# Optimization experiments

Hardware: AMD Instinct MI355X
Metric: run time of the kernel (lower is better)

## Reference

```python
import jax, jax.numpy as jnp
import numpy as np

N_NODES = 100000
N_EDGES = 3200000
IN_FEAT = 128
IN_ENC = 128
HID = 256
MPNN_STEPS = 4


def setup_inputs() -> dict:
    key = jax.random.key(0)
    ks = jax.random.split(key, 12)
    x = jax.random.normal(ks[0], (N_NODES, IN_FEAT), dtype=jnp.float32)
    edge_index = jax.random.randint(ks[1], (2, N_EDGES), 0, N_NODES, dtype=jnp.int64)
    # input layer
    W_in = jax.random.normal(ks[2], (IN_ENC, IN_FEAT), dtype=jnp.float32) * (1.0 / np.sqrt(IN_FEAT))
    b_in = jax.random.normal(ks[3], (IN_ENC,), dtype=jnp.float32) * 0.01
    # MGU params (torch.randn init)
    W_f = jax.random.normal(ks[4], (HID, HID), dtype=jnp.float32)
    U_f = jax.random.normal(ks[5], (HID, HID), dtype=jnp.float32)
    b_f = jax.random.normal(ks[6], (HID,), dtype=jnp.float32)
    W_h = jax.random.normal(ks[7], (HID, HID), dtype=jnp.float32)
    U_h = jax.random.normal(ks[8], (HID, HID), dtype=jnp.float32)
    b_h = jax.random.normal(ks[9], (HID,), dtype=jnp.float32)
    # prediction layer
    W_pred = jax.random.normal(ks[10], (1, HID), dtype=jnp.float32) * (1.0 / np.sqrt(HID))
    b_pred = jax.random.normal(ks[11], (1,), dtype=jnp.float32) * 0.01
    return {"x": x, "edge_index": edge_index, "W_in": W_in, "b_in": b_in,
            "W_f": W_f, "U_f": U_f, "b_f": b_f, "W_h": W_h, "U_h": U_h, "b_h": b_h,
            "W_pred": W_pred, "b_pred": b_pred}


def _mgu_update(m, h, W_f, U_f, b_f, W_h, U_h, b_h):
    # f_t = sigmoid(m @ W_f^T + h @ U_f^T + b_f)
    f_t = jax.nn.sigmoid(m @ W_f.T + h @ U_f.T + b_f)
    h_hat = jnp.tanh(m @ W_h.T + (f_t * h) @ U_h.T + b_h)
    return (1.0 - f_t) * h + f_t * h_hat


def reference(x, edge_index, W_in, b_in, W_f, U_f, b_f, W_h, U_h, b_h, W_pred, b_pred):
    # input encoding
    h0 = jax.nn.relu(x @ W_in.T + b_in)
    # zero-pad features from IN_ENC to HID
    h = jnp.pad(h0, ((0, 0), (0, HID - IN_ENC)))
    src, dst = edge_index[0], edge_index[1]
    for _ in range(MPNN_STEPS):
        # gather neighbor (source) features, scatter-mean to destination nodes
        msg_sum = jax.ops.segment_sum(h[src], dst, num_segments=N_NODES)
        cnt = jax.ops.segment_sum(jnp.ones((src.shape[0],), dtype=h.dtype), dst,
                                  num_segments=N_NODES)
        m = msg_sum / jnp.maximum(cnt, 1.0)[:, None]
        h = _mgu_update(m, h, W_f, U_f, b_f, W_h, U_h, b_h)
    # graph-level readout: per-feature mean over nodes
    g = jnp.mean(h, axis=0)  # [HID]
    return g @ W_pred.T + b_pred  # [1]
```

## Files before the change

kernel.cpp:

```cpp
#include <hip/hip_runtime.h>
#include <hip/hip_bf16.h>
#include <math.h>

constexpr int NN = 100000;
constexpr int NE = 3200000;
constexpr int HID = 256;
constexpr int NBLK = (NN + 255) / 256;

typedef __attribute__((ext_vector_type(8))) short short8;
typedef __attribute__((ext_vector_type(4))) float floatx4;
typedef __attribute__((ext_vector_type(2))) float floatx2;
typedef __attribute__((ext_vector_type(8))) unsigned short ushort8v;

__device__ __forceinline__ float bf2f(unsigned short u) {
    unsigned int t = ((unsigned int)u) << 16;
    float f; __builtin_memcpy(&f, &t, 4); return f;
}
__device__ __forceinline__ unsigned short f2bf(float f) {
    unsigned int t; __builtin_memcpy(&t, &f, 4);
    unsigned int lsb = (t >> 16) & 1u;
    t += 0x7fffu + lsb;
    return (unsigned short)(t >> 16);
}
__device__ __forceinline__ unsigned char f2fp8(float f) {
    int pk = __builtin_amdgcn_cvt_pk_fp8_f32(f, f, 0, false);
    return (unsigned char)(pk & 0xff);
}

__device__ __forceinline__ void llds16(const void* g, void* l) {
    __builtin_amdgcn_global_load_lds(
        (const __attribute__((address_space(1))) unsigned int*)g,
        (__attribute__((address_space(3))) unsigned int*)l, 16, 0, 0);
}

__global__ void detect_i64(const int* __restrict__ ei, int* __restrict__ flag) {
    if (blockIdx.x == 0 && threadIdx.x == 0) {
        int z = 1;
        for (int i = 0; i < 64; ++i)
            if (ei[2 * i + 1] != 0) { z = 0; break; }
        *flag = z;
    }
}
__device__ __forceinline__ int load_edge(const int* ei, int is64, long long idx) {
    if (is64) return (int)(((const long long*)ei)[idx]);
    return ei[idx];
}

__global__ void zero_setup(int* __restrict__ cnt, int* __restrict__ cursor,
                           float* __restrict__ gsum) {
    int i = blockIdx.x * 256 + threadIdx.x;
    if (i < NN) { cnt[i] = 0; cursor[i] = 0; }
    if (i < HID) gsum[i] = 0.0f;
}

__global__ void conv_weights(const float* __restrict__ Wf, const float* __restrict__ Uf,
                             const float* __restrict__ Wh, const float* __restrict__ Uh,
                             const float* __restrict__ Win,
                             unsigned short* __restrict__ wcf,
                             unsigned short* __restrict__ wch,
                             unsigned short* __restrict__ wib) {
    int i = blockIdx.x * 256 + threadIdx.x;
    if (i < 256 * 512) {
        int n = i >> 9, k = i & 511;
        float vf = (k < 256) ? Wf[n * 256 + k] : Uf[n * 256 + k - 256];
        float vh = (k < 256) ? Wh[n * 256 + k] : Uh[n * 256 + k - 256];
        wcf[i] = f2bf(vf); wch[i] = f2bf(vh);
    }
    if (i < 128 * 128) wib[i] = f2bf(Win[i]);
}

__global__ void conv_x(const float* __restrict__ x, unsigned short* __restrict__ xb) {
    int i = blockIdx.x * 256 + threadIdx.x;
    if (i < NN * 128 / 4) {
        float4 v = ((const float4*)x)[i];
        ushort4 o;
        o.x = f2bf(v.x); o.y = f2bf(v.y); o.z = f2bf(v.z); o.w = f2bf(v.w);
        ((ushort4*)xb)[i] = o;
    }
}

__global__ void count_deg(const int* __restrict__ ei, const int* __restrict__ flag,
                          int* __restrict__ cnt) {
    int e = blockIdx.x * 256 + threadIdx.x;
    if (e >= NE) return;
    int is64 = *flag;
    int d = load_edge(ei, is64, (long long)NE + e);
    d = min(max(d, 0), NN - 1);
    atomicAdd(&cnt[d], 1);
}

__global__ void scan_k1(const int* __restrict__ cnt, int* __restrict__ loc,
                        int* __restrict__ bsum) {
    __shared__ int s[256];
    int b = blockIdx.x, t = threadIdx.x;
    int i = b * 256 + t;
    int v = (i < NN) ? cnt[i] : 0;
    s[t] = v;
    __syncthreads();
    for (int ofs = 1; ofs < 256; ofs <<= 1) {
        int tv = (t >= ofs) ? s[t - ofs] : 0;
        __syncthreads();
        s[t] += tv;
        __syncthreads();
    }
    if (i < NN) loc[i] = s[t] - v;
    if (t == 255) bsum[b] = s[255];
}
__global__ void scan_k2(const int* __restrict__ bsum, int* __restrict__ bpre) {
    __shared__ int s[512];
    int t = threadIdx.x;
    int v = (t < NBLK) ? bsum[t] : 0;
    s[t] = v;
    __syncthreads();
    for (int ofs = 1; ofs < 512; ofs <<= 1) {
        int tv = (t >= ofs) ? s[t - ofs] : 0;
        __syncthreads();
        s[t] += tv;
        __syncthreads();
    }
    if (t < NBLK) bpre[t] = s[t] - v;
    if (t == NBLK - 1) bpre[NBLK] = s[t];
}
__global__ void scan_k3(const int* __restrict__ loc, const int* __restrict__ bpre,
                        int* __restrict__ off) {
    int b = blockIdx.x, t = threadIdx.x;
    int i = b * 256 + t;
    if (i < NN) off[i] = loc[i] + bpre[b];
    if (b == 0 && t == 0) off[NN] = bpre[NBLK];
}

__global__ void fill_csr(const int* __restrict__ ei, const int* __restrict__ flag,
                         const int* __restrict__ off, int* __restrict__ cursor,
                         int* __restrict__ csr) {
    int e = blockIdx.x * 256 + threadIdx.x;
    if (e >= NE) return;
    int is64 = *flag;
    int s = load_edge(ei, is64, e);
    int d = load_edge(ei, is64, (long long)NE + e);
    s = min(max(s, 0), NN - 1);
    d = min(max(d, 0), NN - 1);
    int p = atomicAdd(&cursor[d], 1);
    csr[off[d] + p] = s;
}

__device__ __forceinline__ void acc16(floatx2 (&a)[8], uint4 v) {
    unsigned int d[4] = {v.x, v.y, v.z, v.w};
#pragma unroll
    for (int q = 0; q < 4; ++q) {
        floatx2 lo = __builtin_amdgcn_cvt_pk_f32_fp8(d[q], false);
        floatx2 hi = __builtin_amdgcn_cvt_pk_f32_fp8(d[q], true);
        a[q * 2 + 0] += lo;
        a[q * 2 + 1] += hi;
    }
}

__global__ __launch_bounds__(256)
void agg8(const unsigned char* __restrict__ hq, const int* __restrict__ off,
          const int* __restrict__ csr, unsigned short* __restrict__ m) {
    int node = blockIdx.x * 4 + (threadIdx.x >> 6);
    int lane = threadIdx.x & 63;
    int eslot = lane >> 3;
    int fl = lane & 7;
    int fbase = blockIdx.y * 128;
    int e0 = off[node], e1 = off[node + 1];
    const unsigned char* hp = hq + fbase + fl * 16;
    floatx2 a0[8], a1[8];
#pragma unroll
    for (int k = 0; k < 8; ++k) {
        a0[k][0] = 0.f; a0[k][1] = 0.f;
        a1[k][0] = 0.f; a1[k][1] = 0.f;
    }
    int e = e0;
    for (; e + 16 <= e1; e += 16) {
        int s0 = csr[e + eslot];
        int s1 = csr[e + 8 + eslot];
        uint4 v0 = *(const uint4*)(hp + (size_t)s0 * 256);
        uint4 v1 = *(const uint4*)(hp + (size_t)s1 * 256);
        acc16(a0, v0);
        acc16(a1, v1);
    }
    for (; e + 8 <= e1; e += 8) {
        int s0 = csr[e + eslot];
        uint4 v0 = *(const uint4*)(hp + (size_t)s0 * 256);
        acc16(a0, v0);
    }
    if (e + eslot < e1) {
        int s0 = csr[e + eslot];
        uint4 v0 = *(const uint4*)(hp + (size_t)s0 * 256);
        acc16(a1, v0);
    }
#pragma unroll
    for (int k = 0; k < 8; ++k) a0[k] += a1[k];
#pragma unroll
    for (int k = 0; k < 8; ++k) {
#pragma unroll
        for (int c = 0; c < 2; ++c) {
            a0[k][c] += __shfl_xor(a0[k][c], 8, 64);
            a0[k][c] += __shfl_xor(a0[k][c], 16, 64);
            a0[k][c] += __shfl_xor(a0[k][c], 32, 64);
        }
    }
    float inv = 1.0f / (float)max(e1 - e0, 1);
    if (eslot == 0) {
        ushort8v o0, o1;
#pragma unroll
        for (int k = 0; k < 8; ++k) {
            o0[k] = f2bf(a0[k >> 1][k & 1] * inv);
            o1[k] = f2bf(a0[4 + (k >> 1)][k & 1] * inv);
        }
        unsigned short* mp = m + (size_t)node * HID + fbase + fl * 16;
        *(ushort8v*)mp = o0;
        *(ushort8v*)(mp + 8) = o1;
    }
}

template <int MODE>
__global__ __launch_bounds__(256)
void gemm_mfma(const unsigned short* __restrict__ A0,
               const unsigned short* __restrict__ A1,
               const unsigned short* __restrict__ Bw,
               const float* __restrict__ bias,
               unsigned short* Out,
               unsigned char* Hq) {
    constexpr int KTOT = 128;
    constexpr int ASTR = 256;
    constexpr int BSTR = 256;

    __shared__ unsigned short As[128 * 32];
    __shared__ unsigned short Bs[128 * 32];

    const int tid = threadIdx.x;
    const int wave = tid >> 6, lane = tid & 63;
    const int wr = (wave >> 1) * 64, wc = (wave & 1) * 64;
    const int lq = lane >> 4, lm = lane & 15;
    const int rowBase = blockIdx.x * 128;
    const int colBase = 0;

    floatx4 acc[4][4];
#pragma unroll
    for (int i = 0; i < 4; ++i)
#pragma unroll
        for (int j = 0; j < 4; ++j) {
            acc[i][j][0] = 0.f; acc[i][j][1] = 0.f;
            acc[i][j][2] = 0.f; acc[i][j][3] = 0.f;
        }

    for (int k0 = 0; k0 < KTOT; k0 += 32) {
        const unsigned short* Ak = A0;
        int kc = k0;
#pragma unroll
        for (int q = 0; q < 2; ++q) {
            int id = wave * 128 + q * 64 + lane;
            int r = id >> 2, c = id & 3;
            int grow = rowBase + r;
            if (grow > NN - 1) grow = NN - 1;
            const char* ga = (const char*)Ak + (size_t)grow * ASTR + kc * 2 + c * 16;
            char* la = (char*)As + (size_t)(wave * 128 + q * 64) * 16;
            llds16(ga, la);
            const char* gb = (const char*)Bw + (size_t)(colBase + r) * BSTR + k0 * 2 + c * 16;
            char* lb = (char*)Bs + (size_t)(wave * 128 + q * 64) * 16;
            llds16(gb, lb);
        }
        __syncthreads();
        short8 af[4], bf_[4];
#pragma unroll
        for (int i = 0; i < 4; ++i)
            af[i] = *(const short8*)&As[(wr + i * 16 + lm) * 32 + lq * 8];
#pragma unroll
        for (int j = 0; j < 4; ++j)
            bf_[j] = *(const short8*)&Bs[(wc + j * 16 + lm) * 32 + lq * 8];
#pragma unroll
        for (int i = 0; i < 4; ++i)
#pragma unroll
            for (int j = 0; j < 4; ++j)
                acc[i][j] = __builtin_amdgcn_mfma_f32_16x16x32_bf16(
                    af[i], bf_[j], acc[i][j], 0, 0, 0);
        __syncthreads();
    }

#pragma unroll
    for (int i = 0; i < 4; ++i) {
#pragma unroll
        for (int r = 0; r < 4; ++r) {
            int row = rowBase + wr + i * 16 + lq * 4 + r;
            if (row >= NN) continue;
            size_t rb = (size_t)row * HID;
#pragma unroll
            for (int j = 0; j < 4; ++j) {
                int col = colBase + wc + j * 16 + lm;
                float v = acc[i][j][r] + bias[col];
                float rv = fmaxf(v, 0.f);
                Out[rb + col] = f2bf(rv);
                Out[rb + col + 128] = 0;
                Hq[rb + col] = f2fp8(rv);
                Hq[rb + col + 128] = 0;
            }
        }
    }
}

template <int MODE>
__global__ __launch_bounds__(512, 4)
void gemm_wide(const unsigned short* __restrict__ A0,
               const unsigned short* __restrict__ A1,
               const unsigned short* __restrict__ Bw,
               const float* __restrict__ bias,
               const unsigned short* Hh,
               unsigned short* Ff,
               unsigned short* HF,
               unsigned short* Out,
               unsigned char* Hq) {
    constexpr int ASTR = 512;
    constexpr int BSTR = 1024;

    __shared__ unsigned short As[128 * 32];
    __shared__ unsigned short Bs[256 * 32];

    const int tid = threadIdx.x;
    const int wave = tid >> 6, lane = tid & 63;
    const int wr = (wave >> 2) * 64, wc = (wave & 3) * 64;
    const int lq = lane >> 4, lm = lane & 15;
    const int rowBase = blockIdx.x * 128;

    floatx4 acc[4][4];
#pragma unroll
    for (int i = 0; i < 4; ++i)
#pragma unroll
        for (int j = 0; j < 4; ++j) {
            acc[i][j][0] = 0.f; acc[i][j][1] = 0.f;
            acc[i][j][2] = 0.f; acc[i][j][3] = 0.f;
        }

    for (int k0 = 0; k0 < 512; k0 += 32) {
        const unsigned short* Ak = (k0 >= 256) ? A1 : A0;
        const int kc = (k0 >= 256) ? k0 - 256 : k0;
        {
            int r = tid >> 2, c = tid & 3;
            int grow = rowBase + r;
            if (grow > NN - 1) grow = NN - 1;
            llds16((const char*)Ak + (size_t)grow * ASTR + kc * 2 + c * 16,
                   (char*)As + (size_t)wave * 1024);
        }
#pragma unroll
        for (int q = 0; q < 2; ++q) {
            int id = wave * 128 + q * 64 + lane;
            int r = id >> 2, c = id & 3;
            llds16((const char*)Bw + (size_t)r * BSTR + k0 * 2 + c * 16,
                   (char*)Bs + (size_t)(wave * 128 + q * 64) * 16);
        }
        __syncthreads();
        short8 af[4], bf_[4];
#pragma unroll
        for (int i = 0; i < 4; ++i)
            af[i] = *(const short8*)&As[(wr + i * 16 + lm) * 32 + lq * 8];
#pragma unroll
        for (int j = 0; j < 4; ++j)
            bf_[j] = *(const short8*)&Bs[(wc + j * 16 + lm) * 32 + lq * 8];
#pragma unroll
        for (int i = 0; i < 4; ++i)
#pragma unroll
            for (int j = 0; j < 4; ++j)
                acc[i][j] = __builtin_amdgcn_mfma_f32_16x16x32_bf16(
                    af[i], bf_[j], acc[i][j], 0, 0, 0);
        __syncthreads();
    }

#pragma unroll
    for (int i = 0; i < 4; ++i) {
#pragma unroll
        for (int r = 0; r < 4; ++r) {
            int row = rowBase + wr + i * 16 + lq * 4 + r;
            if (row >= NN) continue;
            size_t rb = (size_t)row * HID;
#pragma unroll
            for (int j = 0; j < 4; ++j) {
                int col = wc + j * 16 + lm;
                float v = acc[i][j][r] + bias[col];
                if (MODE == 1) {
                    float f = 1.f / (1.f + __expf(-v));
                    float hv = bf2f(Hh[rb + col]);
                    Ff[rb + col] = f2bf(f);
                    HF[rb + col] = f2bf(f * hv);
                } else {
                    float xc = fminf(fmaxf(v, -12.f), 12.f);
                    float e2 = __expf(2.f * xc);
                    float t = (e2 - 1.f) / (e2 + 1.f);
                    float f = bf2f(Ff[rb + col]);
                    float hv = bf2f(Hh[rb + col]);
                    float nh = (1.f - f) * hv + f * t;
                    Out[rb + col] = f2bf(nh);
                    Hq[rb + col] = f2fp8(nh);
                }
            }
        }
    }
}

__global__ __launch_bounds__(256)
void colmean(const unsigned short* __restrict__ h, float* __restrict__ gsum) {
    int j = threadIdx.x;
    long long n0 = (long long)blockIdx.x * 256;
    float acc = 0.0f;
    for (int n = 0; n < 256; ++n) {
        long long node = n0 + n;
        if (node < NN) acc += bf2f(h[node * HID + j]);
    }
    atomicAdd(&gsum[j], acc);
}

__global__ __launch_bounds__(256)
void final_pred(const float* __restrict__ gsum, const float* __restrict__ Wp,
                const float* __restrict__ bp, float* __restrict__ out) {
    __shared__ float s[256];
    int j = threadIdx.x;
    s[j] = gsum[j] * (1.0f / (float)NN) * Wp[j];
    __syncthreads();
    for (int ofs = 128; ofs > 0; ofs >>= 1) {
        if (j < ofs) s[j] += s[j + ofs];
        __syncthreads();
    }
    if (j == 0) out[0] = s[0] + bp[0];
}

extern "C" void kernel_launch(void* const* d_in, const int* in_sizes, int n_in,
                              void* d_out, int out_size, void* d_ws, size_t ws_size,
                              hipStream_t stream) {
    const float* x      = (const float*)d_in[0];
    const int*   ei     = (const int*)d_in[1];
    const float* W_in   = (const float*)d_in[2];
    const float* b_in   = (const float*)d_in[3];
    const float* W_f    = (const float*)d_in[4];
    const float* U_f    = (const float*)d_in[5];
    const float* b_f    = (const float*)d_in[6];
    const float* W_h    = (const float*)d_in[7];
    const float* U_h    = (const float*)d_in[8];
    const float* b_h    = (const float*)d_in[9];
    const float* W_pred = (const float*)d_in[10];
    const float* b_pred = (const float*)d_in[11];
    float* out = (float*)d_out;

    char* p = (char*)d_ws;
    auto alloc = [&](size_t bytes) {
        char* r = p;
        p += (bytes + 511) & ~(size_t)511;
        return r;
    };
    int*            cnt    = (int*)alloc((size_t)NN * 4);
    int*            cursor = (int*)alloc((size_t)NN * 4);
    int*            off    = (int*)alloc((size_t)(NN + 1) * 4);
    int*            flag   = (int*)alloc(4);
    float*          gsum   = (float*)alloc(HID * 4);
    int*            loc    = (int*)alloc((size_t)NN * 4);
    int*            bsum   = (int*)alloc((size_t)NBLK * 4);
    int*            bpre   = (int*)alloc((size_t)(NBLK + 1) * 4);
    unsigned short* wcf    = (unsigned short*)alloc((size_t)256 * 512 * 2);
    unsigned short* wch    = (unsigned short*)alloc((size_t)256 * 512 * 2);
    unsigned short* wib    = (unsigned short*)alloc((size_t)128 * 128 * 2);
    int*            csr    = (int*)alloc((size_t)NE * 4);
    unsigned short* hbuf   = (unsigned short*)alloc((size_t)NN * HID * 2);
    unsigned short* mbuf   = (unsigned short*)alloc((size_t)NN * HID * 2);
    unsigned short* fbuf   = (unsigned short*)alloc((size_t)NN * HID * 2);
    unsigned short* hf     = (unsigned short*)alloc((size_t)NN * HID * 2);
    unsigned char*  hq     = (unsigned char*)alloc((size_t)NN * HID);
    unsigned short* xb     = hf;

    detect_i64<<<1, 64, 0, stream>>>(ei, flag);
    zero_setup<<<NBLK, 256, 0, stream>>>(cnt, cursor, gsum);
    conv_weights<<<512, 256, 0, stream>>>(W_f, U_f, W_h, U_h, W_in, wcf, wch, wib);
    conv_x<<<(NN * 128 / 4 + 255) / 256, 256, 0, stream>>>(x, xb);

    count_deg<<<(NE + 255) / 256, 256, 0, stream>>>(ei, flag, cnt);
    scan_k1<<<NBLK, 256, 0, stream>>>(cnt, loc, bsum);
    scan_k2<<<1, 512, 0, stream>>>(bsum, bpre);
    scan_k3<<<NBLK, 256, 0, stream>>>(loc, bpre, off);
    fill_csr<<<(NE + 255) / 256, 256, 0, stream>>>(ei, flag, off, cursor, csr);

    const int MBLK = (NN + 127) / 128;
    gemm_mfma<0><<<dim3(MBLK, 1), 256, 0, stream>>>(
        xb, nullptr, wib, b_in, hbuf, hq);

    for (int step = 0; step < 4; ++step) {
        agg8<<<dim3(NN / 4, 2), 256, 0, stream>>>(hq, off, csr, mbuf);
        gemm_wide<1><<<dim3(MBLK, 1), 512, 0, stream>>>(
            mbuf, hbuf, wcf, b_f, hbuf, fbuf, hf, nullptr, nullptr);
        gemm_wide<2><<<dim3(MBLK, 1), 512, 0, stream>>>(
            mbuf, hf, wch, b_h, hbuf, fbuf, nullptr, hbuf, hq);
    }

    colmean<<<NBLK, 256, 0, stream>>>(hbuf, gsum);
    final_pred<<<1, 256, 0, stream>>>(gsum, W_pred, b_pred, out);
}
```

Before: 1.693 ms.

## Fuse MGU gate and candidate GEMMs into one kernel with LDS-resident f*h

Merges the two per-step MGU GEMM kernels into a single kernel over 64-row tiles. The forget gate is computed first, kept packed in registers, and f*h is staged in shared memory as the A operand for the second GEMM. This removes the global round trips for the f and f*h buffers and one launch per step. In exchange each block reloads the full 256-wide weight tile for both GEMMs over a smaller row tile, uses more shared memory, and has higher register pressure, which may lower occupancy.

```diff
diff --git a/kernel.cpp b/kernel.cpp
--- a/kernel.cpp
+++ b/kernel.cpp
@@ -214,18 +214,12 @@
     }
 }
 
-template <int MODE>
 __global__ __launch_bounds__(256)
-void gemm_mfma(const unsigned short* __restrict__ A0,
-               const unsigned short* __restrict__ A1,
-               const unsigned short* __restrict__ Bw,
-               const float* __restrict__ bias,
-               unsigned short* Out,
-               unsigned char* Hq) {
-    constexpr int KTOT = 128;
-    constexpr int ASTR = 256;
-    constexpr int BSTR = 256;
-
+void gemm_encode(const unsigned short* __restrict__ A0,
+                 const unsigned short* __restrict__ Bw,
+                 const float* __restrict__ bias,
+                 unsigned short* Out,
+                 unsigned char* Hq) {
     __shared__ unsigned short As[128 * 32];
     __shared__ unsigned short Bs[128 * 32];
 
@@ -234,7 +228,6 @@
     const int wr = (wave >> 1) * 64, wc = (wave & 1) * 64;
     const int lq = lane >> 4, lm = lane & 15;
     const int rowBase = blockIdx.x * 128;
-    const int colBase = 0;
 
     floatx4 acc[4][4];
 #pragma unroll
@@ -245,21 +238,17 @@
             acc[i][j][2] = 0.f; acc[i][j][3] = 0.f;
         }
 
-    for (int k0 = 0; k0 < KTOT; k0 += 32) {
-        const unsigned short* Ak = A0;
-        int kc = k0;
+    for (int k0 = 0; k0 < 128; k0 += 32) {
 #pragma unroll
         for (int q = 0; q < 2; ++q) {
             int id = wave * 128 + q * 64 + lane;
             int r = id >> 2, c = id & 3;
             int grow = rowBase + r;
             if (grow > NN - 1) grow = NN - 1;
-            const char* ga = (const char*)Ak + (size_t)grow * ASTR + kc * 2 + c * 16;
-            char* la = (char*)As + (size_t)(wave * 128 + q * 64) * 16;
-            llds16(ga, la);
-            const char* gb = (const char*)Bw + (size_t)(colBase + r) * BSTR + k0 * 2 + c * 16;
-            char* lb = (char*)Bs + (size_t)(wave * 128 + q * 64) * 16;
-            llds16(gb, lb);
+            llds16((const char*)A0 + (size_t)grow * 256 + k0 * 2 + c * 16,
+                   (char*)As + (size_t)(wave * 128 + q * 64) * 16);
+            llds16((const char*)Bw + (size_t)r * 256 + k0 * 2 + c * 16,
+                   (char*)Bs + (size_t)(wave * 128 + q * 64) * 16);
         }
         __syncthreads();
         short8 af[4], bf_[4];
@@ -287,7 +276,7 @@
             size_t rb = (size_t)row * HID;
 #pragma unroll
             for (int j = 0; j < 4; ++j) {
-                int col = colBase + wc + j * 16 + lm;
+                int col = wc + j * 16 + lm;
                 float v = acc[i][j][r] + bias[col];
                 float rv = fmaxf(v, 0.f);
                 Out[rb + col] = f2bf(rv);
@@ -299,28 +288,23 @@
     }
 }
 
-template <int MODE>
-__global__ __launch_bounds__(512, 4)
-void gemm_wide(const unsigned short* __restrict__ A0,
-               const unsigned short* __restrict__ A1,
-               const unsigned short* __restrict__ Bw,
-               const float* __restrict__ bias,
-               const unsigned short* Hh,
-               unsigned short* Ff,
-               unsigned short* HF,
-               unsigned short* Out,
-               unsigned char* Hq) {
-    constexpr int ASTR = 512;
-    constexpr int BSTR = 1024;
-
-    __shared__ unsigned short As[128 * 32];
+__global__ __launch_bounds__(256, 3)
+void mgu_fused(const unsigned short* __restrict__ M,
+               unsigned short* Hio,
+               const unsigned short* __restrict__ Wfc,
+               const unsigned short* __restrict__ Whc,
+               const float* __restrict__ bf_bias,
+               const float* __restrict__ bh_bias,
+               unsigned char* __restrict__ Hq) {
+    __shared__ unsigned short As[64 * 32];
     __shared__ unsigned short Bs[256 * 32];
+    __shared__ unsigned short FHs[64 * 264];
 
     const int tid = threadIdx.x;
-    const int wave = tid >> 6, lane = tid & 63;
-    const int wr = (wave >> 2) * 64, wc = (wave & 3) * 64;
+    const int lane = tid & 63;
+    const int wc = (tid >> 6) * 64;
     const int lq = lane >> 4, lm = lane & 15;
-    const int rowBase = blockIdx.x * 128;
+    const int rowBase = blockIdx.x * 64;
 
     floatx4 acc[4][4];
 #pragma unroll
@@ -332,65 +316,129 @@
         }
 
     for (int k0 = 0; k0 < 512; k0 += 32) {
-        const unsigned short* Ak = (k0 >= 256) ? A1 : A0;
-        const int kc = (k0 >= 256) ? k0 - 256 : k0;
+        const unsigned short* Ak = (k0 >= 256) ? Hio : M;
+        const int kc = k0 & 255;
         {
             int r = tid >> 2, c = tid & 3;
             int grow = rowBase + r;
             if (grow > NN - 1) grow = NN - 1;
-            llds16((const char*)Ak + (size_t)grow * ASTR + kc * 2 + c * 16,
-                   (char*)As + (size_t)wave * 1024);
-        }
-#pragma unroll
-        for (int q = 0; q < 2; ++q) {
-            int id = wave * 128 + q * 64 + lane;
+            llds16((const char*)Ak + (size_t)grow * 512 + kc * 2 + c * 16,
+                   (char*)As + (size_t)tid * 16);
+        }
+#pragma unroll
+        for (int q = 0; q < 4; ++q) {
+            int id = q * 256 + tid;
             int r = id >> 2, c = id & 3;
-            llds16((const char*)Bw + (size_t)r * BSTR + k0 * 2 + c * 16,
-                   (char*)Bs + (size_t)(wave * 128 + q * 64) * 16);
-        }
-        __syncthreads();
-        short8 af[4], bf_[4];
+            llds16((const char*)Wfc + (size_t)r * 1024 + k0 * 2 + c * 16,
+                   (char*)Bs + (size_t)id * 16);
+        }
+        __syncthreads();
+        short8 af[4], bfr[4];
 #pragma unroll
         for (int i = 0; i < 4; ++i)
-            af[i] = *(const short8*)&As[(wr + i * 16 + lm) * 32 + lq * 8];
+            af[i] = *(const short8*)&As[(i * 16 + lm) * 32 + lq * 8];
 #pragma unroll
         for (int j = 0; j < 4; ++j)
-            bf_[j] = *(const short8*)&Bs[(wc + j * 16 + lm) * 32 + lq * 8];
+            bfr[j] = *(const short8*)&Bs[(wc + j * 16 + lm) * 32 + lq * 8];
 #pragma unroll
         for (int i = 0; i < 4; ++i)
 #pragma unroll
             for (int j = 0; j < 4; ++j)
                 acc[i][j] = __builtin_amdgcn_mfma_f32_16x16x32_bf16(
-                    af[i], bf_[j], acc[i][j], 0, 0, 0);
-        __syncthreads();
-    }
-
+                    af[i], bfr[j], acc[i][j], 0, 0, 0);
+        __syncthreads();
+    }
+
+    unsigned int f_pk[4][4][2];
 #pragma unroll
     for (int i = 0; i < 4; ++i) {
 #pragma unroll
-        for (int r = 0; r < 4; ++r) {
-            int row = rowBase + wr + i * 16 + lq * 4 + r;
-            if (row >= NN) continue;
-            size_t rb = (size_t)row * HID;
-#pragma unroll
-            for (int j = 0; j < 4; ++j) {
-                int col = wc + j * 16 + lm;
-                float v = acc[i][j][r] + bias[col];
-                if (MODE == 1) {
-                    float f = 1.f / (1.f + __expf(-v));
-                    float hv = bf2f(Hh[rb + col]);
-                    Ff[rb + col] = f2bf(f);
-                    HF[rb + col] = f2bf(f * hv);
-                } else {
-                    float xc = fminf(fmaxf(v, -12.f), 12.f);
-                    float e2 = __expf(2.f * xc);
-                    float t = (e2 - 1.f) / (e2 + 1.f);
-                    float f = bf2f(Ff[rb + col]);
-                    float hv = bf2f(Hh[rb + col]);
-                    float nh = (1.f - f) * hv + f * t;
-                    Out[rb + col] = f2bf(nh);
-                    Hq[rb + col] = f2fp8(nh);
-                }
+        for (int j = 0; j < 4; ++j) {
+            int col = wc + j * 16 + lm;
+            float bb = bf_bias[col];
+#pragma unroll
+            for (int r = 0; r < 4; ++r) {
+                int row_t = i * 16 + lq * 4 + r;
+                int row = rowBase + row_t;
+                float f = 1.f / (1.f + __expf(-(acc[i][j][r] + bb)));
+                unsigned int fb = f2bf(f);
+                if (r == 0)      f_pk[i][j][0] = fb;
+                else if (r == 1) f_pk[i][j][0] |= fb << 16;
+                else if (r == 2) f_pk[i][j][1] = fb;
+                else             f_pk[i][j][1] |= fb << 16;
+                float hv = (row < NN) ? bf2f(Hio[(size_t)row * HID + col]) : 0.f;
+                FHs[row_t * 264 + col] = f2bf(f * hv);
+            }
+        }
+    }
+    __syncthreads();
+
+#pragma unroll
+    for (int i = 0; i < 4; ++i)
+#pragma unroll
+        for (int j = 0; j < 4; ++j) {
+            acc[i][j][0] = 0.f; acc[i][j][1] = 0.f;
+            acc[i][j][2] = 0.f; acc[i][j][3] = 0.f;
+        }
+    for (int k0 = 0; k0 < 512; k0 += 32) {
+        if (k0 < 256) {
+            int r = tid >> 2, c = tid & 3;
+            int grow = rowBase + r;
+            if (grow > NN - 1) grow = NN - 1;
+            llds16((const char*)M + (size_t)grow * 512 + k0 * 2 + c * 16,
+                   (char*)As + (size_t)tid * 16);
+        }
+#pragma unroll
+        for (int q = 0; q < 4; ++q) {
+            int id = q * 256 + tid;
+            int r = id >> 2, c = id & 3;
+            llds16((const char*)Whc + (size_t)r * 1024 + k0 * 2 + c * 16,
+                   (char*)Bs + (size_t)id * 16);
+        }
+        __syncthreads();
+        short8 af[4], bfr[4];
+        if (k0 < 256) {
+#pragma unroll
+            for (int i = 0; i < 4; ++i)
+                af[i] = *(const short8*)&As[(i * 16 + lm) * 32 + lq * 8];
+        } else {
+            const int kc = k0 - 256;
+#pragma unroll
+            for (int i = 0; i < 4; ++i)
+                af[i] = *(const short8*)&FHs[(i * 16 + lm) * 264 + kc + lq * 8];
+        }
+#pragma unroll
+        for (int j = 0; j < 4; ++j)
+            bfr[j] = *(const short8*)&Bs[(wc + j * 16 + lm) * 32 + lq * 8];
+#pragma unroll
+        for (int i = 0; i < 4; ++i)
+#pragma unroll
+            for (int j = 0; j < 4; ++j)
+                acc[i][j] = __builtin_amdgcn_mfma_f32_16x16x32_bf16(
+                    af[i], bfr[j], acc[i][j], 0, 0, 0);
+        __syncthreads();
+    }
+
+#pragma unroll
+    for (int i = 0; i < 4; ++i) {
+#pragma unroll
+        for (int j = 0; j < 4; ++j) {
+            int col = wc + j * 16 + lm;
+            float bb = bh_bias[col];
+#pragma unroll
+            for (int r = 0; r < 4; ++r) {
+                int row = rowBase + i * 16 + lq * 4 + r;
+                if (row >= NN) continue;
+                size_t rb = (size_t)row * HID;
+                float v = acc[i][j][r] + bb;
+                float xc = fminf(fmaxf(v, -12.f), 12.f);
+                float e2 = __expf(2.f * xc);
+                float t = (e2 - 1.f) / (e2 + 1.f);
+                float f = bf2f((unsigned short)((f_pk[i][j][r >> 1] >> ((r & 1) * 16)) & 0xffffu));
+                float hv = bf2f(Hio[rb + col]);
+                float nh = (1.f - f) * hv + f * t;
+                Hio[rb + col] = f2bf(nh);
+                Hq[rb + col] = f2fp8(nh);
             }
         }
     }
@@ -459,10 +507,8 @@
     int*            csr    = (int*)alloc((size_t)NE * 4);
     unsigned short* hbuf   = (unsigned short*)alloc((size_t)NN * HID * 2);
     unsigned short* mbuf   = (unsigned short*)alloc((size_t)NN * HID * 2);
-    unsigned short* fbuf   = (unsigned short*)alloc((size_t)NN * HID * 2);
-    unsigned short* hf     = (unsigned short*)alloc((size_t)NN * HID * 2);
     unsigned char*  hq     = (unsigned char*)alloc((size_t)NN * HID);
-    unsigned short* xb     = hf;
+    unsigned short* xb     = mbuf;
 
     detect_i64<<<1, 64, 0, stream>>>(ei, flag);
     zero_setup<<<NBLK, 256, 0, stream>>>(cnt, cursor, gsum);
@@ -475,16 +521,14 @@
     scan_k3<<<NBLK, 256, 0, stream>>>(loc, bpre, off);
     fill_csr<<<(NE + 255) / 256, 256, 0, stream>>>(ei, flag, off, cursor, csr);
 
-    const int MBLK = (NN + 127) / 128;
-    gemm_mfma<0><<<dim3(MBLK, 1), 256, 0, stream>>>(
-        xb, nullptr, wib, b_in, hbuf, hq);
-
+    gemm_encode<<<dim3((NN + 127) / 128), 256, 0, stream>>>(
+        xb, wib, b_in, hbuf, hq);
+
+    const int FBLK = (NN + 63) / 64;
     for (int step = 0; step < 4; ++step) {
         agg8<<<dim3(NN / 4, 2), 256, 0, stream>>>(hq, off, csr, mbuf);
-        gemm_wide<1><<<dim3(MBLK, 1), 512, 0, stream>>>(
-            mbuf, hbuf, wcf, b_f, hbuf, fbuf, hf, nullptr, nullptr);
-        gemm_wide<2><<<dim3(MBLK, 1), 512, 0, stream>>>(
-            mbuf, hf, wch, b_h, hbuf, fbuf, nullptr, hbuf, hq);
+        mgu_fused<<<dim3(FBLK), 256, 0, stream>>>(
+            mbuf, hbuf, wcf, wch, b_f, b_h, hq);
     }
 
     colmean<<<NBLK, 256, 0, stream>>>(hbuf, gsum);
```

Measured after the change: 1.956 ms. 15.6% more time.

## Double-buffer LDS in gemm_wide and stage epilogue through LDS for vector stores

Applied to the files above, without the earlier changes.

The gemm_wide K loop now uses two LDS buffers: the next K tile is prefetched with direct-to-LDS loads while MFMAs run on the current one, using explicit vmcnt waits and raw barriers in place of two full __syncthreads per iteration. The epilogue first writes the activated tile to LDS, 64 rows at a time. It then reads it back row-contiguously, so loads and stores of Ff, HF, Out and Hq become 16-byte vectors instead of scattered 2-byte and 1-byte accesses. Shared memory per block grows to about 48KB, which may cap blocks per CU below the launch-bounds target. The encoder GEMM is also simplified into a non-templated kernel.

```diff
diff --git a/kernel.cpp b/kernel.cpp
--- a/kernel.cpp
+++ b/kernel.cpp
@@ -214,18 +214,12 @@
     }
 }
 
-template <int MODE>
 __global__ __launch_bounds__(256)
-void gemm_mfma(const unsigned short* __restrict__ A0,
-               const unsigned short* __restrict__ A1,
-               const unsigned short* __restrict__ Bw,
-               const float* __restrict__ bias,
-               unsigned short* Out,
-               unsigned char* Hq) {
-    constexpr int KTOT = 128;
-    constexpr int ASTR = 256;
-    constexpr int BSTR = 256;
-
+void gemm_encode(const unsigned short* __restrict__ A0,
+                 const unsigned short* __restrict__ Bw,
+                 const float* __restrict__ bias,
+                 unsigned short* Out,
+                 unsigned char* Hq) {
     __shared__ unsigned short As[128 * 32];
     __shared__ unsigned short Bs[128 * 32];
 
@@ -234,7 +228,6 @@
     const int wr = (wave >> 1) * 64, wc = (wave & 1) * 64;
     const int lq = lane >> 4, lm = lane & 15;
     const int rowBase = blockIdx.x * 128;
-    const int colBase = 0;
 
     floatx4 acc[4][4];
 #pragma unroll
@@ -245,21 +238,17 @@
             acc[i][j][2] = 0.f; acc[i][j][3] = 0.f;
         }
 
-    for (int k0 = 0; k0 < KTOT; k0 += 32) {
-        const unsigned short* Ak = A0;
-        int kc = k0;
+    for (int k0 = 0; k0 < 128; k0 += 32) {
 #pragma unroll
         for (int q = 0; q < 2; ++q) {
             int id = wave * 128 + q * 64 + lane;
             int r = id >> 2, c = id & 3;
             int grow = rowBase + r;
             if (grow > NN - 1) grow = NN - 1;
-            const char* ga = (const char*)Ak + (size_t)grow * ASTR + kc * 2 + c * 16;
-            char* la = (char*)As + (size_t)(wave * 128 + q * 64) * 16;
-            llds16(ga, la);
-            const char* gb = (const char*)Bw + (size_t)(colBase + r) * BSTR + k0 * 2 + c * 16;
-            char* lb = (char*)Bs + (size_t)(wave * 128 + q * 64) * 16;
-            llds16(gb, lb);
+            llds16((const char*)A0 + (size_t)grow * 256 + k0 * 2 + c * 16,
+                   (char*)As + (size_t)(wave * 128 + q * 64) * 16);
+            llds16((const char*)Bw + (size_t)r * 256 + k0 * 2 + c * 16,
+                   (char*)Bs + (size_t)(wave * 128 + q * 64) * 16);
         }
         __syncthreads();
         short8 af[4], bf_[4];
@@ -287,7 +276,7 @@
             size_t rb = (size_t)row * HID;
 #pragma unroll
             for (int j = 0; j < 4; ++j) {
-                int col = colBase + wc + j * 16 + lm;
+                int col = wc + j * 16 + lm;
                 float v = acc[i][j][r] + bias[col];
                 float rv = fmaxf(v, 0.f);
                 Out[rb + col] = f2bf(rv);
@@ -305,16 +294,12 @@
                const unsigned short* __restrict__ A1,
                const unsigned short* __restrict__ Bw,
                const float* __restrict__ bias,
-               const unsigned short* Hh,
-               unsigned short* Ff,
-               unsigned short* HF,
-               unsigned short* Out,
-               unsigned char* Hq) {
-    constexpr int ASTR = 512;
-    constexpr int BSTR = 1024;
-
-    __shared__ unsigned short As[128 * 32];
-    __shared__ unsigned short Bs[256 * 32];
+               const unsigned short* __restrict__ Hh,
+               unsigned short* __restrict__ Ff,
+               unsigned short* __restrict__ HF,
+               unsigned short* __restrict__ Out,
+               unsigned char* __restrict__ Hq) {
+    __shared__ unsigned short SH[2][12288];
 
     const int tid = threadIdx.x;
     const int wave = tid >> 6, lane = tid & 63;
@@ -322,6 +307,10 @@
     const int lq = lane >> 4, lm = lane & 15;
     const int rowBase = blockIdx.x * 128;
 
+    const int ac = tid & 3;
+    int agrow = rowBase + (tid >> 2);
+    if (agrow > NN - 1) agrow = NN - 1;
+
     floatx4 acc[4][4];
 #pragma unroll
     for (int i = 0; i < 4; ++i)
@@ -331,65 +320,105 @@
             acc[i][j][2] = 0.f; acc[i][j][3] = 0.f;
         }
 
-    for (int k0 = 0; k0 < 512; k0 += 32) {
+    auto stage = [&](int b, int k0) {
         const unsigned short* Ak = (k0 >= 256) ? A1 : A0;
-        const int kc = (k0 >= 256) ? k0 - 256 : k0;
-        {
-            int r = tid >> 2, c = tid & 3;
-            int grow = rowBase + r;
-            if (grow > NN - 1) grow = NN - 1;
-            llds16((const char*)Ak + (size_t)grow * ASTR + kc * 2 + c * 16,
-                   (char*)As + (size_t)wave * 1024);
-        }
+        const int kc = k0 & 255;
+        llds16((const char*)Ak + (size_t)agrow * 512 + kc * 2 + ac * 16,
+               (char*)&SH[b][0] + wave * 1024);
 #pragma unroll
         for (int q = 0; q < 2; ++q) {
             int id = wave * 128 + q * 64 + lane;
-            int r = id >> 2, c = id & 3;
-            llds16((const char*)Bw + (size_t)r * BSTR + k0 * 2 + c * 16,
-                   (char*)Bs + (size_t)(wave * 128 + q * 64) * 16);
-        }
-        __syncthreads();
-        short8 af[4], bf_[4];
+            llds16((const char*)Bw + (size_t)(id >> 2) * 1024 + k0 * 2 + (id & 3) * 16,
+                   (char*)&SH[b][4096] + (wave * 128 + q * 64) * 16);
+        }
+    };
+
+    stage(0, 0);
+    for (int ks = 0; ks < 16; ++ks) {
+        const int b = ks & 1;
+        if (ks < 15) {
+            stage(b ^ 1, (ks + 1) * 32);
+            asm volatile("s_waitcnt vmcnt(3)" ::: "memory");
+        } else {
+            asm volatile("s_waitcnt vmcnt(0)" ::: "memory");
+        }
+        __builtin_amdgcn_s_barrier();
+        __builtin_amdgcn_sched_barrier(0);
+        short8 af[4], bfr[4];
 #pragma unroll
         for (int i = 0; i < 4; ++i)
-            af[i] = *(const short8*)&As[(wr + i * 16 + lm) * 32 + lq * 8];
+            af[i] = *(const short8*)&SH[b][(wr + i * 16 + lm) * 32 + lq * 8];
 #pragma unroll
         for (int j = 0; j < 4; ++j)
-            bf_[j] = *(const short8*)&Bs[(wc + j * 16 + lm) * 32 + lq * 8];
+            bfr[j] = *(const short8*)&SH[b][4096 + (wc + j * 16 + lm) * 32 + lq * 8];
 #pragma unroll
         for (int i = 0; i < 4; ++i)
 #pragma unroll
             for (int j = 0; j < 4; ++j)
                 acc[i][j] = __builtin_amdgcn_mfma_f32_16x16x32_bf16(
-                    af[i], bf_[j], acc[i][j], 0, 0, 0);
-        __syncthreads();
-    }
-
-#pragma unroll
-    for (int i = 0; i < 4; ++i) {
-#pragma unroll
-        for (int r = 0; r < 4; ++r) {
-            int row = rowBase + wr + i * 16 + lq * 4 + r;
-            if (row >= NN) continue;
-            size_t rb = (size_t)row * HID;
+                    af[i], bfr[j], acc[i][j], 0, 0, 0);
+        __builtin_amdgcn_sched_barrier(0);
+        __builtin_amdgcn_s_barrier();
+    }
+
+    unsigned short* BB = &SH[0][0];
+    const int lrow = tid >> 3, lcolb = (tid & 7) * 32;
+#pragma unroll
+    for (int c = 0; c < 2; ++c) {
+        __syncthreads();
+        if ((wave >> 2) == c) {
 #pragma unroll
             for (int j = 0; j < 4; ++j) {
-                int col = wc + j * 16 + lm;
-                float v = acc[i][j][r] + bias[col];
+                const int col = wc + j * 16 + lm;
+                const float bb = bias[col];
+#pragma unroll
+                for (int i = 0; i < 4; ++i)
+#pragma unroll
+                    for (int r = 0; r < 4; ++r) {
+                        float v = acc[i][j][r] + bb;
+                        float w = (MODE == 1) ? (1.f / (1.f + __expf(-v))) : v;
+                        BB[(i * 16 + lq * 4 + r) * 264 + col] = f2bf(w);
+                    }
+            }
+        }
+        __syncthreads();
+        const int grow = rowBase + c * 64 + lrow;
+        if (grow < NN) {
+            const size_t rb = (size_t)grow * HID;
+#pragma unroll
+            for (int q = 0; q < 4; ++q) {
+                const int col = lcolb + q * 8;
+                ushort8v wv = *(const ushort8v*)&BB[lrow * 264 + col];
                 if (MODE == 1) {
-                    float f = 1.f / (1.f + __expf(-v));
-                    float hv = bf2f(Hh[rb + col]);
-                    Ff[rb + col] = f2bf(f);
-                    HF[rb + col] = f2bf(f * hv);
+                    ushort8v hv = *(const ushort8v*)&Hh[rb + col];
+                    ushort8v fh;
+#pragma unroll
+                    for (int k = 0; k < 8; ++k)
+                        fh[k] = f2bf(bf2f(wv[k]) * bf2f(hv[k]));
+                    *(ushort8v*)&Ff[rb + col] = wv;
+                    *(ushort8v*)&HF[rb + col] = fh;
                 } else {
-                    float xc = fminf(fmaxf(v, -12.f), 12.f);
-                    float e2 = __expf(2.f * xc);
-                    float t = (e2 - 1.f) / (e2 + 1.f);
-                    float f = bf2f(Ff[rb + col]);
-                    float hv = bf2f(Hh[rb + col]);
-                    float nh = (1.f - f) * hv + f * t;
-                    Out[rb + col] = f2bf(nh);
-                    Hq[rb + col] = f2fp8(nh);
+                    ushort8v fv = *(const ushort8v*)&Ff[rb + col];
+                    ushort8v hv = *(const ushort8v*)&Hh[rb + col];
+                    ushort8v nh8;
+                    unsigned int w0 = 0, w1 = 0;
+#pragma unroll
+                    for (int k = 0; k < 8; ++k) {
+                        float v = bf2f(wv[k]);
+                        float xc = fminf(fmaxf(v, -12.f), 12.f);
+                        float e2 = __expf(2.f * xc);
+                        float t = (e2 - 1.f) / (e2 + 1.f);
+                        float f = bf2f(fv[k]);
+                        float hvv = bf2f(hv[k]);
+                        float nh = (1.f - f) * hvv + f * t;
+                        nh8[k] = f2bf(nh);
+                        unsigned int b8 = f2fp8(nh);
+                        if (k < 4) w0 |= b8 << (k * 8);
+                        else       w1 |= b8 << ((k - 4) * 8);
+                    }
+                    *(ushort8v*)&Out[rb + col] = nh8;
+                    uint2 hqv; hqv.x = w0; hqv.y = w1;
+                    *(uint2*)&Hq[rb + col] = hqv;
                 }
             }
         }
@@ -476,14 +505,13 @@
     fill_csr<<<(NE + 255) / 256, 256, 0, stream>>>(ei, flag, off, cursor, csr);
 
     const int MBLK = (NN + 127) / 128;
-    gemm_mfma<0><<<dim3(MBLK, 1), 256, 0, stream>>>(
-        xb, nullptr, wib, b_in, hbuf, hq);
+    gemm_encode<<<dim3(MBLK), 256, 0, stream>>>(xb, wib, b_in, hbuf, hq);
 
     for (int step = 0; step < 4; ++step) {
         agg8<<<dim3(NN / 4, 2), 256, 0, stream>>>(hq, off, csr, mbuf);
-        gemm_wide<1><<<dim3(MBLK, 1), 512, 0, stream>>>(
+        gemm_wide<1><<<dim3(MBLK), 512, 0, stream>>>(
             mbuf, hbuf, wcf, b_f, hbuf, fbuf, hf, nullptr, nullptr);
-        gemm_wide<2><<<dim3(MBLK, 1), 512, 0, stream>>>(
+        gemm_wide<2><<<dim3(MBLK), 512, 0, stream>>>(
             mbuf, hf, wch, b_h, hbuf, fbuf, nullptr, hbuf, hq);
     }
 
```

Result: slower. 1.778 ms (+5.1%).
